# Optimization experiments

Hardware: AMD Instinct MI355X
Metric: run time of the kernel (lower is better)

## Reference

```python
import jax, jax.numpy as jnp
import numpy as np

IN, H, OUT, T, B = 132, 1024, 132, 100, 256


def setup_inputs() -> dict:
    key = jax.random.key(0)
    ks = jax.random.split(key, 16)
    s_in = 1.0 / np.sqrt(H)
    def mk(k, shape):
        return jax.random.uniform(k, shape, jnp.float32, -s_in, s_in)
    inp = {
        "real_seq": jax.random.normal(ks[0], (B, T, IN), jnp.float32),
        "W_ih1": mk(ks[1], (4 * H, IN)), "W_hh1": mk(ks[2], (4 * H, H)),
        "b_ih1": mk(ks[3], (4 * H,)),   "b_hh1": mk(ks[4], (4 * H,)),
        "W_ih2": mk(ks[5], (4 * H, H)), "W_hh2": mk(ks[6], (4 * H, H)),
        "b_ih2": mk(ks[7], (4 * H,)),   "b_hh2": mk(ks[8], (4 * H,)),
        "W_ih3": mk(ks[9], (4 * H, H)), "W_hh3": mk(ks[10], (4 * H, H)),
        "b_ih3": mk(ks[11], (4 * H,)),  "b_hh3": mk(ks[12], (4 * H,)),
        "W_dec": mk(ks[13], (OUT, H)),  "b_dec": mk(ks[14], (OUT,)),
        "condition_num": 5, "groundtruth_num": 5,
    }
    return inp


def _lstm_cell(x, h, c, W_ih, W_hh, b_ih, b_hh):
    # torch LSTMCell: gates in (i, f, g, o) order
    gates = x @ W_ih.T + b_ih + h @ W_hh.T + b_hh
    i, f, g, o = jnp.split(gates, 4, axis=-1)
    i, f, o = jax.nn.sigmoid(i), jax.nn.sigmoid(f), jax.nn.sigmoid(o)
    g = jnp.tanh(g)
    c_new = f * c + i * g
    h_new = o * jnp.tanh(c_new)
    return h_new, c_new


def reference(real_seq, W_ih1, W_hh1, b_ih1, b_hh1,
              W_ih2, W_hh2, b_ih2, b_hh2,
              W_ih3, W_hh3, b_ih3, b_hh3,
              W_dec, b_dec, condition_num, groundtruth_num):
    batch, seq_len, _ = real_seq.shape
    # static teacher-forcing schedule: [1]*gt_num + [0]*cond_num, tiled
    gt = np.ones((100, groundtruth_num)); con = np.zeros((100, condition_num))
    cond = jnp.asarray(np.concatenate((gt, con), 1).reshape(-1)[:seq_len] == 1)

    z = jnp.zeros((batch, H), jnp.float32)
    init = (z, z, z, z, z, z, jnp.zeros((batch, OUT), jnp.float32))

    def step(carry, xs):
        h0, h1, h2, c0, c1, c2, prev_out = carry
        frame, use_gt = xs
        x = jnp.where(use_gt, frame, prev_out)
        # note: lstm2/lstm3 consume the OLD h0/h1, faithful to forward_lstm
        nh0, nc0 = _lstm_cell(x,  h0, c0, W_ih1, W_hh1, b_ih1, b_hh1)
        nh1, nc1 = _lstm_cell(h0, h1, c1, W_ih2, W_hh2, b_ih2, b_hh2)
        nh2, nc2 = _lstm_cell(h1, h2, c2, W_ih3, W_hh3, b_ih3, b_hh3)
        out = nh2 @ W_dec.T + b_dec
        return (nh0, nh1, nh2, nc0, nc1, nc2, out), out

    xs = (jnp.swapaxes(real_seq, 0, 1), cond)  # [T,B,IN], [T]
    _, outs = jax.lax.scan(step, init, xs)      # outs: [T,B,OUT]
    # torch concatenates along dim 1 each step -> [B, T*OUT]
    return jnp.swapaxes(outs, 0, 1).reshape(batch, seq_len * OUT)
```

## Files before the change

### kernel.cpp

```cpp
#include <hip/hip_runtime.h>
#include <math.h>

#define B_   256
#define T_   100
#define IN_  132
#define OUT_ 132
#define H_   1024
#define BH   ((size_t)B_ * H_)

typedef _Float16 f16;
typedef _Float16 f16x8 __attribute__((ext_vector_type(8)));
typedef float    f32x4 __attribute__((ext_vector_type(4)));

#define MFMA16(a, b, c) __builtin_amdgcn_mfma_f32_16x16x32_f16((a), (b), (c), 0, 0, 0)

#define AS1 __attribute__((address_space(1)))
#define AS3 __attribute__((address_space(3)))

__device__ __forceinline__ void gl_lds16(const void* g, void* l) {
    __builtin_amdgcn_global_load_lds((AS1 void*)g, (AS3 void*)l, 16, 0, 0);
}

__device__ __forceinline__ float sigmoidf_(float x) {
    return 1.0f / (1.0f + __expf(-x));
}
__device__ __forceinline__ float tanhf_(float x) {
    float e = __expf(2.0f * x);
    return 1.0f - 2.0f / (e + 1.0f);
}


__global__ void conv_pad(const float* __restrict__ src, f16* __restrict__ dst,
                         int src_rows, int src_k, int dst_k) {
    int k = blockIdx.x * 256 + threadIdx.x;
    int r = blockIdx.y;
    if (k >= dst_k) return;
    float v = (r < src_rows && k < src_k) ? src[(size_t)r * src_k + k] : 0.0f;
    dst[(size_t)r * dst_k + k] = (f16)v;
}

__global__ void convT_kernel(const float* __restrict__ Wd, f16* __restrict__ WdT) {
    int k = blockIdx.x * 256 + threadIdx.x;
    int m = blockIdx.y;
    if (k >= 160) return;
    float v = (k < IN_) ? Wd[(size_t)k * H_ + m] : 0.0f;
    WdT[(size_t)m * 160 + k] = (f16)v;
}

__global__ void bias_add_kernel(const float* __restrict__ a, const float* __restrict__ b,
                                float* __restrict__ dst, int n) {
    int i = blockIdx.x * 256 + threadIdx.x;
    if (i < n) dst[i] = a[i] + b[i];
}

__global__ void bfb_kernel(const float* __restrict__ Wih1, const float* __restrict__ bd,
                           float* __restrict__ bfb) {
    int j = blockIdx.x * 256 + threadIdx.x;
    if (j >= 4096) return;
    float s = 0.0f;
    for (int k = 0; k < IN_; ++k) s += Wih1[(size_t)j * IN_ + k] * bd[k];
    bfb[j] = s;
}

__global__ void zero_kernel(float* __restrict__ p, int n) {
    int i = blockIdx.x * blockDim.x + threadIdx.x;
    int st = gridDim.x * blockDim.x;
    for (; i < n; i += st) p[i] = 0.0f;
}

__global__ __launch_bounds__(256) void pack_w(const float* __restrict__ W,
                                              f16* __restrict__ Wpk, int wsel) {
    int jt = blockIdx.x, kt = blockIdx.y;
    f16* dst = Wpk + (((size_t)wsel * 32 + jt) * 32 + kt) * 4096;
    for (int u = threadIdx.x; u < 512; u += 256) {
        int c = u >> 2, ch = u & 3;
        int gate = (c >> 4) & 3, jj = (c & 15) + (c >> 6) * 16;
        const float* s = W + ((size_t)gate * 1024 + jt * 32 + jj) * 1024 + kt * 32 + ch * 8;
        f16x8 v;
#pragma unroll
        for (int e = 0; e < 8; ++e) v[e] = (f16)s[e];
        *(f16x8*)(dst + (size_t)u * 8) = v;
    }
}

__global__ __launch_bounds__(256) void pack_wf16(const f16* __restrict__ W,
                                                 f16* __restrict__ Wpk, int wsel) {
    int jt = blockIdx.x, kt = blockIdx.y;
    f16* dst = Wpk + (((size_t)wsel * 32 + jt) * 32 + kt) * 4096;
    for (int u = threadIdx.x; u < 512; u += 256) {
        int c = u >> 2, ch = u & 3;
        int gate = (c >> 4) & 3, jj = (c & 15) + (c >> 6) * 16;
        const f16* s = W + ((size_t)gate * 1024 + jt * 32 + jj) * 1024 + kt * 32 + ch * 8;
        f16x8 v = *(const f16x8*)s;
        *(f16x8*)(dst + (size_t)u * 8) = v;
    }
}

__global__ __launch_bounds__(256) void pack_w0(const float* __restrict__ W,
                                               f16* __restrict__ W0pk) {
    int jt = blockIdx.x, kt = blockIdx.y;
    f16* dst = W0pk + ((size_t)jt * 5 + kt) * 4096;
    for (int u = threadIdx.x; u < 512; u += 256) {
        int c = u >> 2, ch = u & 3;
        int gate = (c >> 4) & 3, jj = (c & 15) + (c >> 6) * 16;
        int row = gate * 1024 + jt * 32 + jj;
        f16x8 v;
#pragma unroll
        for (int e = 0; e < 8; ++e) {
            int k = kt * 32 + ch * 8 + e;
            v[e] = (f16)((k < IN_) ? W[(size_t)row * IN_ + k] : 0.0f);
        }
        *(f16x8*)(dst + (size_t)u * 8) = v;
    }
}

__global__ __launch_bounds__(256) void pack_seq(const float* __restrict__ seq,
                                                f16* __restrict__ seqpk) {
    int kt = blockIdx.x, t = blockIdx.y;
    int b = threadIdx.x;
    f16* d = seqpk + (((size_t)t * 5 + kt) * 256 + b) * 32;
#pragma unroll
    for (int ch = 0; ch < 4; ++ch) {
        f16x8 v;
#pragma unroll
        for (int e = 0; e < 8; ++e) {
            int k = kt * 32 + ch * 8 + e;
            v[e] = (f16)((k < IN_) ? seq[((size_t)b * T_ + t) * IN_ + k] : 0.0f);
        }
        *(f16x8*)(d + ch * 8) = v;
    }
}

__global__ __launch_bounds__(256) void wfb_mfma(
    const f16* __restrict__ W0, const f16* __restrict__ WdT, f16* __restrict__ Wfb)
{
    const int m0 = blockIdx.x * 128;
    const int n0 = blockIdx.y * 128;
    const int tid  = threadIdx.x;
    const int lane = tid & 63;
    const int w    = tid >> 6;
    const int lx   = lane & 15;
    const int quad = lane >> 4;
    const int wrow = w >> 1, wcol = w & 1;

    __shared__ __align__(16) char lds[32768];

    auto stA = [&](int kt, int buf) {
        char* base = lds + buf * 16384;
#pragma unroll
        for (int i = 0; i < 2; ++i) {
            int r  = w * 32 + i * 16 + (lane >> 2);
            int sg = (lane & 3) ^ (r & 3);
            const f16* g = W0 + (size_t)(m0 + r) * 160 + kt * 32 + sg * 8;
            gl_lds16(g, base + (size_t)(w * 32 + i * 16) * 64);
        }
    };
    auto stB = [&](int kt, int buf) {
        char* base = lds + 8192 + buf * 16384;
#pragma unroll
        for (int i = 0; i < 2; ++i) {
            int r  = w * 32 + i * 16 + (lane >> 2);
            int sg = (lane & 3) ^ (r & 3);
            const f16* g = WdT + (size_t)(n0 + r) * 160 + kt * 32 + sg * 8;
            gl_lds16(g, base + (size_t)(w * 32 + i * 16) * 64);
        }
    };

    f32x4 acc[4][4];
#pragma unroll
    for (int m = 0; m < 4; ++m)
#pragma unroll
        for (int n = 0; n < 4; ++n) acc[m][n] = (f32x4){0.f, 0.f, 0.f, 0.f};

    stA(0, 0); stB(0, 0);
    for (int kt = 0; kt < 5; ++kt) {
        __syncthreads();
        if (kt + 1 < 5) { stA(kt + 1, (kt + 1) & 1); stB(kt + 1, (kt + 1) & 1); }
        const char* bA = lds + (kt & 1) * 16384;
        const char* bB = lds + 8192 + (kt & 1) * 16384;
        f16x8 af[4], bf[4];
#pragma unroll
        for (int m = 0; m < 4; ++m) {
            int R = wrow * 64 + m * 16 + lx;
            af[m] = *(const f16x8*)(bA + R * 64 + ((quad ^ (R & 3)) * 16));
        }
#pragma unroll
        for (int n = 0; n < 4; ++n) {
            int R = wcol * 64 + n * 16 + lx;
            bf[n] = *(const f16x8*)(bB + R * 64 + ((quad ^ (R & 3)) * 16));
        }
#pragma unroll
        for (int m = 0; m < 4; ++m)
#pragma unroll
            for (int n = 0; n < 4; ++n)
                acc[m][n] = MFMA16(af[m], bf[n], acc[m][n]);
    }

#pragma unroll
    for (int m = 0; m < 4; ++m)
#pragma unroll
        for (int n = 0; n < 4; ++n)
#pragma unroll
            for (int r = 0; r < 4; ++r) {
                int row = m0 + wrow * 64 + m * 16 + quad * 4 + r;
                int col = n0 + wcol * 64 + n * 16 + lx;
                Wfb[(size_t)row * H_ + col] = (f16)acc[m][n][r];
            }
}

__global__ __launch_bounds__(256) void step_mfma(
    const f16* __restrict__ seqpk,
    const f16* __restrict__ h2pkP,
    const f16* __restrict__ h01pkC,
    f16* __restrict__ h01pkN,
    f16* __restrict__ h2pkN,
    f16* __restrict__ histN,
    float* __restrict__ c_st,
    const f16* __restrict__ W0pk,
    const f16* __restrict__ Wpk,
    const float* __restrict__ bias_comb,
    const float* __restrict__ bfb,
    const int* __restrict__ cnum, const int* __restrict__ gnum,
    int t)
{
    const int jt   = blockIdx.x;
    const int mb   = blockIdx.y;
    const int l    = blockIdx.z;
    const int tid  = threadIdx.x;
    const int lane = tid & 63;
    const int w    = tid >> 6;
    const int lx   = lane & 15;
    const int quad = lane >> 4;
    const int wrow = w >> 1, wcol = w & 1;

    __shared__ __align__(16) char lds[49152];

    bool use_gt = false;
    int n0 = 32;
    const char *A0 = nullptr, *B0 = nullptr;
    const char* wb = (const char*)Wpk + (size_t)jt * 262144;
    if (l == 0) {
        int cn = cnum[0], gn = gnum[0];
        use_gt = (t % (cn + gn)) < gn;
        if (use_gt)      { A0 = (const char*)(seqpk + (size_t)t * 5 * 8192);
                           B0 = (const char*)(W0pk + (size_t)jt * 5 * 4096); n0 = 5; }
        else if (t == 0) { n0 = 0; }
        else             { A0 = (const char*)h2pkP; B0 = wb + (size_t)5 * 8388608; }
    } else if (l == 1) { A0 = (const char*)h01pkC;        B0 = wb + (size_t)1 * 8388608; }
    else               { A0 = (const char*)(h01pkC + BH); B0 = wb + (size_t)3 * 8388608; }
    const char* A1 = (l == 0) ? (const char*)h01pkC
                   : (l == 1) ? (const char*)(h01pkC + BH) : (const char*)h2pkP;
    const char* B1 = wb + (size_t)((l == 0) ? 0 : (l == 1) ? 2 : 4) * 8388608;
    const int ntot = n0 + 32;

    const int lr = lane >> 2, lc = lane & 3;
    const int perl = lr * 64 + ((lc ^ (lr & 3)) * 16);

    auto stage = [&](int kt, int buf) {
        const char *pA, *pB; int kk;
        if (kt < n0) { kk = kt;      pA = A0; pB = B0; }
        else         { kk = kt - n0; pA = A1; pB = B1; }
        char* base = lds + buf * 12288;
        gl_lds16(pA + (size_t)kk * 16384 + (size_t)(mb * 64 + w * 16) * 64 + perl,
                 base + w * 1024);
#pragma unroll
        for (int i = 0; i < 2; ++i)
            gl_lds16(pB + (size_t)kk * 8192 + (size_t)(w * 2 + i) * 1024 + perl,
                     base + 4096 + (size_t)(w * 2 + i) * 1024);
    };

    f32x4 acc[2][4];
#pragma unroll
    for (int m = 0; m < 2; ++m)
#pragma unroll
        for (int n = 0; n < 4; ++n) acc[m][n] = (f32x4){0.f, 0.f, 0.f, 0.f};

    stage(0, 0);
    stage(1, 1);
    stage(2, 2);

    for (int kt = 0; kt < ntot; ++kt) {
        if (kt < ntot - 2)       asm volatile("s_waitcnt vmcnt(6)" ::: "memory");
        else if (kt == ntot - 2) asm volatile("s_waitcnt vmcnt(3)" ::: "memory");
        else                     asm volatile("s_waitcnt vmcnt(0)" ::: "memory");
        __builtin_amdgcn_s_barrier();

        const char* bA = lds + (kt & 3) * 12288;
        const char* bB = bA + 4096;
        f16x8 af[2], bf[4];
#pragma unroll
        for (int m = 0; m < 2; ++m) {
            int R = wrow * 32 + m * 16 + lx;
            af[m] = *(const f16x8*)(bA + R * 64 + ((quad ^ (R & 3)) * 16));
        }
#pragma unroll
        for (int n = 0; n < 4; ++n) {
            int R = wcol * 64 + n * 16 + lx;
            bf[n] = *(const f16x8*)(bB + R * 64 + ((quad ^ (R & 3)) * 16));
        }
        asm volatile("s_waitcnt lgkmcnt(0)" ::: "memory");
        __builtin_amdgcn_sched_barrier(0);
        __builtin_amdgcn_s_barrier();

        if (kt + 3 < ntot) stage(kt + 3, (kt + 3) & 3);

        __builtin_amdgcn_s_setprio(1);
#pragma unroll
        for (int m = 0; m < 2; ++m)
#pragma unroll
            for (int n = 0; n < 4; ++n)
                acc[m][n] = MFMA16(af[m], bf[n], acc[m][n]);
        __builtin_amdgcn_s_setprio(0);
    }

    const int j = jt * 32 + wcol * 16 + lx;
    const float* bc = bias_comb + l * 4096;
    const bool addfb = (l == 0 && !use_gt && t > 0);
    float bi  = bc[j]        + (addfb ? bfb[j]        : 0.f);
    float bff = bc[1024 + j] + (addfb ? bfb[1024 + j] : 0.f);
    float bg  = bc[2048 + j] + (addfb ? bfb[2048 + j] : 0.f);
    float bo  = bc[3072 + j] + (addfb ? bfb[3072 + j] : 0.f);
#pragma unroll
    for (int m = 0; m < 2; ++m) {
#pragma unroll
        for (int r = 0; r < 4; ++r) {
            int b = mb * 64 + wrow * 32 + m * 16 + quad * 4 + r;
            float gi = acc[m][0][r] + bi;
            float gf = acc[m][1][r] + bff;
            float gg = acc[m][2][r] + bg;
            float go = acc[m][3][r] + bo;
            size_t ix = ((size_t)l * B_ + b) * H_ + j;
            float cn = sigmoidf_(gf) * c_st[ix] + sigmoidf_(gi) * tanhf_(gg);
            c_st[ix] = cn;
            float hv = sigmoidf_(go) * tanhf_(cn);
            f16 hv16 = (f16)hv;
            size_t pix = ((size_t)(j >> 5) * 256 + b) * 32 + (j & 31);
            if (l == 2) { h2pkN[pix] = hv16; histN[(size_t)b * H_ + j] = hv16; }
            else        h01pkN[(size_t)l * BH + pix] = hv16;
        }
    }
}

__global__ __launch_bounds__(256) void decode_mfma(
    const f16* __restrict__ hist,
    const f16* __restrict__ Wd16,
    const float* __restrict__ bd,
    float* __restrict__ dout)
{
    const int r0  = blockIdx.x * 128;
    const int nb0 = blockIdx.y * 32;
    const int tid  = threadIdx.x;
    const int lane = tid & 63;
    const int w    = tid >> 6;
    const int lx   = lane & 15;
    const int quad = lane >> 4;

    __shared__ __align__(16) char lds[20480];

    auto stA = [&](int kt, int buf) {
        char* base = lds + buf * 10240;
#pragma unroll
        for (int i = 0; i < 2; ++i) {
            int r  = w * 32 + i * 16 + (lane >> 2);
            int sg = (lane & 3) ^ (r & 3);
            const f16* g = hist + (size_t)(r0 + r) * H_ + kt * 32 + sg * 8;
            gl_lds16(g, base + (size_t)(w * 32 + i * 16) * 64);
        }
    };
    auto stB = [&](int kt, int buf) {
        char* base = lds + 8192 + buf * 10240;
        if (w < 2) {
            int r  = w * 16 + (lane >> 2);
            int sg = (lane & 3) ^ (r & 3);
            const f16* g = Wd16 + (size_t)(nb0 + r) * H_ + kt * 32 + sg * 8;
            gl_lds16(g, base + (size_t)(w * 16) * 64);
        }
    };

    f32x4 acc[2][2];
#pragma unroll
    for (int m = 0; m < 2; ++m)
#pragma unroll
        for (int n = 0; n < 2; ++n) acc[m][n] = (f32x4){0.f, 0.f, 0.f, 0.f};

    stA(0, 0); stB(0, 0);
    for (int kt = 0; kt < 32; ++kt) {
        __syncthreads();
        if (kt + 1 < 32) { stA(kt + 1, (kt + 1) & 1); stB(kt + 1, (kt + 1) & 1); }
        const char* bA = lds + (kt & 1) * 10240;
        const char* bB = lds + 8192 + (kt & 1) * 10240;
        f16x8 af[2], bf[2];
#pragma unroll
        for (int m = 0; m < 2; ++m) {
            int R = w * 32 + m * 16 + lx;
            af[m] = *(const f16x8*)(bA + R * 64 + ((quad ^ (R & 3)) * 16));
        }
#pragma unroll
        for (int n = 0; n < 2; ++n) {
            int R = n * 16 + lx;
            bf[n] = *(const f16x8*)(bB + R * 64 + ((quad ^ (R & 3)) * 16));
        }
#pragma unroll
        for (int m = 0; m < 2; ++m)
#pragma unroll
            for (int n = 0; n < 2; ++n)
                acc[m][n] = MFMA16(af[m], bf[n], acc[m][n]);
    }

#pragma unroll
    for (int n = 0; n < 2; ++n) {
        int nn = nb0 + n * 16 + lx;
        if (nn < OUT_) {
            float bv = bd[nn];
#pragma unroll
            for (int m = 0; m < 2; ++m)
#pragma unroll
                for (int r = 0; r < 4; ++r) {
                    int row = r0 + w * 32 + m * 16 + quad * 4 + r;
                    int tt = row >> 8, b = row & 255;
                    dout[(size_t)b * (T_ * OUT_) + (size_t)tt * OUT_ + nn] = acc[m][n][r] + bv;
                }
        }
    }
}


extern "C" void kernel_launch(void* const* d_in, const int* in_sizes, int n_in,
                              void* d_out, int out_size, void* d_ws, size_t ws_size,
                              hipStream_t stream) {
    const float* seq  = (const float*)d_in[0];
    const float* Wih1 = (const float*)d_in[1];
    const float* Whh1 = (const float*)d_in[2];
    const float* bih1 = (const float*)d_in[3];
    const float* bhh1 = (const float*)d_in[4];
    const float* Wih2 = (const float*)d_in[5];
    const float* Whh2 = (const float*)d_in[6];
    const float* bih2 = (const float*)d_in[7];
    const float* bhh2 = (const float*)d_in[8];
    const float* Wih3 = (const float*)d_in[9];
    const float* Whh3 = (const float*)d_in[10];
    const float* bih3 = (const float*)d_in[11];
    const float* bhh3 = (const float*)d_in[12];
    const float* Wd   = (const float*)d_in[13];
    const float* bd   = (const float*)d_in[14];
    const int*   cnum = (const int*)d_in[15];
    const int*   gnum = (const int*)d_in[16];

    char* p = (char*)d_ws;
    f16*  W0   = (f16*)p;  p += (size_t)4096 * 160 * 2;
    f16*  Wd16 = (f16*)p;  p += (size_t)160 * 1024 * 2;
    f16*  WdT  = (f16*)p;  p += (size_t)1024 * 160 * 2;
    f16*  Wfb  = (f16*)p;  p += (size_t)4096 * 1024 * 2;
    float* bias_comb = (float*)p; p += (size_t)3 * 4096 * 4;
    float* bfb = (float*)p; p += (size_t)4096 * 4;
    f16*  hist = (f16*)p;  p += (size_t)100 * BH * 2;
    f16*  h01pkA = (f16*)p; p += (size_t)2 * BH * 2;
    f16*  h2pkA  = (f16*)p; p += (size_t)BH * 2;
    float* c_st  = (float*)p; p += (size_t)3 * BH * 4;
    f16*  h01pkB = (f16*)p; p += (size_t)2 * BH * 2;
    f16*  h2pkB  = (f16*)p; p += (size_t)BH * 2;
    f16*  Wpk   = (f16*)p; p += (size_t)6 * 32 * 32 * 4096 * 2;
    f16*  W0pk  = (f16*)p; p += (size_t)32 * 5 * 4096 * 2;
    f16*  seqpk = (f16*)p; p += (size_t)T_ * 5 * 256 * 32 * 2;

    const int zero_floats = (int)(((size_t)3 * BH * 2 + (size_t)3 * BH * 4) / 4);

    conv_pad<<<dim3(1, 4096), 256, 0, stream>>>(Wih1, W0, 4096, IN_, 160);
    conv_pad<<<dim3(4, 160), 256, 0, stream>>>(Wd, Wd16, OUT_, H_, H_);
    convT_kernel<<<dim3(1, 1024), 256, 0, stream>>>(Wd, WdT);
    bias_add_kernel<<<16, 256, 0, stream>>>(bih1, bhh1, bias_comb + 0 * 4096, 4096);
    bias_add_kernel<<<16, 256, 0, stream>>>(bih2, bhh2, bias_comb + 1 * 4096, 4096);
    bias_add_kernel<<<16, 256, 0, stream>>>(bih3, bhh3, bias_comb + 2 * 4096, 4096);
    bfb_kernel<<<16, 256, 0, stream>>>(Wih1, bd, bfb);
    wfb_mfma<<<dim3(32, 8), 256, 0, stream>>>(W0, WdT, Wfb);
    pack_w<<<dim3(32, 32), 256, 0, stream>>>(Whh1, Wpk, 0);
    pack_w<<<dim3(32, 32), 256, 0, stream>>>(Wih2, Wpk, 1);
    pack_w<<<dim3(32, 32), 256, 0, stream>>>(Whh2, Wpk, 2);
    pack_w<<<dim3(32, 32), 256, 0, stream>>>(Wih3, Wpk, 3);
    pack_w<<<dim3(32, 32), 256, 0, stream>>>(Whh3, Wpk, 4);
    pack_wf16<<<dim3(32, 32), 256, 0, stream>>>(Wfb, Wpk, 5);
    pack_w0<<<dim3(32, 5), 256, 0, stream>>>(Wih1, W0pk);
    pack_seq<<<dim3(5, T_), 256, 0, stream>>>(seq, seqpk);
    zero_kernel<<<512, 256, 0, stream>>>((float*)h01pkA, zero_floats);

    f16 *h01C = h01pkA, *h01N = h01pkB, *h2P = h2pkA, *h2N = h2pkB;
    for (int t = 0; t < T_; ++t) {
        step_mfma<<<dim3(32, 4, 3), 256, 0, stream>>>(
            seqpk, h2P, h01C, h01N, h2N, hist + (size_t)t * BH, c_st,
            W0pk, Wpk, bias_comb, bfb, cnum, gnum, t);
        f16* tmp;
        tmp = h01C; h01C = h01N; h01N = tmp;
        tmp = h2P;  h2P  = h2N;  h2N  = tmp;
    }

    decode_mfma<<<dim3(200, 5), 256, 0, stream>>>(hist, Wd16, bd, (float*)d_out);
}
```

Baseline: 3.020 ms.

## Split step kernel K-dimension across two waves with register-direct loads

```diff
diff --git a/kernel.cpp b/kernel.cpp
--- a/kernel.cpp
+++ b/kernel.cpp
@@ -70,48 +70,43 @@
 
 __global__ __launch_bounds__(256) void pack_w(const float* __restrict__ W,
                                               f16* __restrict__ Wpk, int wsel) {
-    int jt = blockIdx.x, kt = blockIdx.y;
-    f16* dst = Wpk + (((size_t)wsel * 32 + jt) * 32 + kt) * 4096;
-    for (int u = threadIdx.x; u < 512; u += 256) {
-        int c = u >> 2, ch = u & 3;
-        int gate = (c >> 4) & 3, jj = (c & 15) + (c >> 6) * 16;
-        const float* s = W + ((size_t)gate * 1024 + jt * 32 + jj) * 1024 + kt * 32 + ch * 8;
-        f16x8 v;
-#pragma unroll
-        for (int e = 0; e < 8; ++e) v[e] = (f16)s[e];
-        *(f16x8*)(dst + (size_t)u * 8) = v;
-    }
+    int jt = blockIdx.x, kk = blockIdx.y;
+    f16* dst = Wpk + (((size_t)wsel * 64 + jt) * 32 + kk) * 2048;
+    int u = threadIdx.x;
+    int c = u >> 2, ch = u & 3;
+    int row = ((c >> 4) & 3) * 1024 + jt * 16 + (c & 15);
+    const float* s = W + (size_t)row * 1024 + kk * 32 + ch * 8;
+    f16x8 v;
+#pragma unroll
+    for (int e = 0; e < 8; ++e) v[e] = (f16)s[e];
+    *(f16x8*)(dst + (size_t)c * 32 + ch * 8) = v;
 }
 
 __global__ __launch_bounds__(256) void pack_wf16(const f16* __restrict__ W,
                                                  f16* __restrict__ Wpk, int wsel) {
-    int jt = blockIdx.x, kt = blockIdx.y;
-    f16* dst = Wpk + (((size_t)wsel * 32 + jt) * 32 + kt) * 4096;
-    for (int u = threadIdx.x; u < 512; u += 256) {
-        int c = u >> 2, ch = u & 3;
-        int gate = (c >> 4) & 3, jj = (c & 15) + (c >> 6) * 16;
-        const f16* s = W + ((size_t)gate * 1024 + jt * 32 + jj) * 1024 + kt * 32 + ch * 8;
-        f16x8 v = *(const f16x8*)s;
-        *(f16x8*)(dst + (size_t)u * 8) = v;
-    }
+    int jt = blockIdx.x, kk = blockIdx.y;
+    f16* dst = Wpk + (((size_t)wsel * 64 + jt) * 32 + kk) * 2048;
+    int u = threadIdx.x;
+    int c = u >> 2, ch = u & 3;
+    int row = ((c >> 4) & 3) * 1024 + jt * 16 + (c & 15);
+    f16x8 v = *(const f16x8*)(W + (size_t)row * 1024 + kk * 32 + ch * 8);
+    *(f16x8*)(dst + (size_t)c * 32 + ch * 8) = v;
 }
 
 __global__ __launch_bounds__(256) void pack_w0(const float* __restrict__ W,
                                                f16* __restrict__ W0pk) {
-    int jt = blockIdx.x, kt = blockIdx.y;
-    f16* dst = W0pk + ((size_t)jt * 5 + kt) * 4096;
-    for (int u = threadIdx.x; u < 512; u += 256) {
-        int c = u >> 2, ch = u & 3;
-        int gate = (c >> 4) & 3, jj = (c & 15) + (c >> 6) * 16;
-        int row = gate * 1024 + jt * 32 + jj;
-        f16x8 v;
-#pragma unroll
-        for (int e = 0; e < 8; ++e) {
-            int k = kt * 32 + ch * 8 + e;
-            v[e] = (f16)((k < IN_) ? W[(size_t)row * IN_ + k] : 0.0f);
-        }
-        *(f16x8*)(dst + (size_t)u * 8) = v;
-    }
+    int jt = blockIdx.x, kk = blockIdx.y;
+    f16* dst = W0pk + ((size_t)jt * 5 + kk) * 2048;
+    int u = threadIdx.x;
+    int c = u >> 2, ch = u & 3;
+    int row = ((c >> 4) & 3) * 1024 + jt * 16 + (c & 15);
+    f16x8 v;
+#pragma unroll
+    for (int e = 0; e < 8; ++e) {
+        int k = kk * 32 + ch * 8 + e;
+        v[e] = (f16)((k < IN_) ? W[(size_t)row * IN_ + k] : 0.0f);
+    }
+    *(f16x8*)(dst + (size_t)c * 32 + ch * 8) = v;
 }
 
 __global__ __launch_bounds__(256) void pack_seq(const float* __restrict__ seq,
@@ -208,7 +203,7 @@
             }
 }
 
-__global__ __launch_bounds__(256) void step_mfma(
+__global__ __launch_bounds__(128) void step_mfma(
     const f16* __restrict__ seqpk,
     const f16* __restrict__ h2pkP,
     const f16* __restrict__ h01pkC,
@@ -231,89 +226,95 @@
     const int w    = tid >> 6;
     const int lx   = lane & 15;
     const int quad = lane >> 4;
-    const int wrow = w >> 1, wcol = w & 1;
-
-    __shared__ __align__(16) char lds[49152];
+
+    __shared__ float ex[2][2][4][4][64];
 
     bool use_gt = false;
     int n0 = 32;
     const char *A0 = nullptr, *B0 = nullptr;
-    const char* wb = (const char*)Wpk + (size_t)jt * 262144;
+    const char* wbase = (const char*)Wpk + (size_t)jt * 131072;
     if (l == 0) {
         int cn = cnum[0], gn = gnum[0];
         use_gt = (t % (cn + gn)) < gn;
-        if (use_gt)      { A0 = (const char*)(seqpk + (size_t)t * 5 * 8192);
-                           B0 = (const char*)(W0pk + (size_t)jt * 5 * 4096); n0 = 5; }
+        if (use_gt)      { A0 = (const char*)(seqpk + (size_t)t * 40960);
+                           B0 = (const char*)(W0pk + (size_t)jt * 10240); n0 = 5; }
         else if (t == 0) { n0 = 0; }
-        else             { A0 = (const char*)h2pkP; B0 = wb + (size_t)5 * 8388608; }
-    } else if (l == 1) { A0 = (const char*)h01pkC;        B0 = wb + (size_t)1 * 8388608; }
-    else               { A0 = (const char*)(h01pkC + BH); B0 = wb + (size_t)3 * 8388608; }
+        else             { A0 = (const char*)h2pkP; B0 = wbase + (size_t)5 * 8388608; }
+    } else if (l == 1) { A0 = (const char*)h01pkC;        B0 = wbase + (size_t)1 * 8388608; }
+    else               { A0 = (const char*)(h01pkC + BH); B0 = wbase + (size_t)3 * 8388608; }
     const char* A1 = (l == 0) ? (const char*)h01pkC
                    : (l == 1) ? (const char*)(h01pkC + BH) : (const char*)h2pkP;
-    const char* B1 = wb + (size_t)((l == 0) ? 0 : (l == 1) ? 2 : 4) * 8388608;
+    const char* B1 = wbase + (size_t)((l == 0) ? 0 : (l == 1) ? 2 : 4) * 8388608;
     const int ntot = n0 + 32;
-
-    const int lr = lane >> 2, lc = lane & 3;
-    const int perl = lr * 64 + ((lc ^ (lr & 3)) * 16);
-
-    auto stage = [&](int kt, int buf) {
-        const char *pA, *pB; int kk;
-        if (kt < n0) { kk = kt;      pA = A0; pB = B0; }
-        else         { kk = kt - n0; pA = A1; pB = B1; }
-        char* base = lds + buf * 12288;
-        gl_lds16(pA + (size_t)kk * 16384 + (size_t)(mb * 64 + w * 16) * 64 + perl,
-                 base + w * 1024);
-#pragma unroll
-        for (int i = 0; i < 2; ++i)
-            gl_lds16(pB + (size_t)kk * 8192 + (size_t)(w * 2 + i) * 1024 + perl,
-                     base + 4096 + (size_t)(w * 2 + i) * 1024);
-    };
-
-    f32x4 acc[2][4];
-#pragma unroll
-    for (int m = 0; m < 2; ++m)
+    const int nh = (ntot + 1) >> 1;
+    const int lo = w ? nh : 0;
+    const int hi = w ? ntot : nh;
+
+    const int aoff = (mb * 64 + lx) * 64 + quad * 16;
+    const int boff = lx * 64 + quad * 16;
+
+    f32x4 acc[4][4];
+#pragma unroll
+    for (int m = 0; m < 4; ++m)
 #pragma unroll
         for (int n = 0; n < 4; ++n) acc[m][n] = (f32x4){0.f, 0.f, 0.f, 0.f};
 
-    stage(0, 0);
-    stage(1, 1);
-    stage(2, 2);
-
-    for (int kt = 0; kt < ntot; ++kt) {
-        if (kt < ntot - 2)       asm volatile("s_waitcnt vmcnt(6)" ::: "memory");
-        else if (kt == ntot - 2) asm volatile("s_waitcnt vmcnt(3)" ::: "memory");
-        else                     asm volatile("s_waitcnt vmcnt(0)" ::: "memory");
-        __builtin_amdgcn_s_barrier();
-
-        const char* bA = lds + (kt & 3) * 12288;
-        const char* bB = bA + 4096;
-        f16x8 af[2], bf[4];
-#pragma unroll
-        for (int m = 0; m < 2; ++m) {
-            int R = wrow * 32 + m * 16 + lx;
-            af[m] = *(const f16x8*)(bA + R * 64 + ((quad ^ (R & 3)) * 16));
-        }
-#pragma unroll
-        for (int n = 0; n < 4; ++n) {
-            int R = wcol * 64 + n * 16 + lx;
-            bf[n] = *(const f16x8*)(bB + R * 64 + ((quad ^ (R & 3)) * 16));
-        }
-        asm volatile("s_waitcnt lgkmcnt(0)" ::: "memory");
-        __builtin_amdgcn_sched_barrier(0);
-        __builtin_amdgcn_s_barrier();
-
-        if (kt + 3 < ntot) stage(kt + 3, (kt + 3) & 3);
-
-        __builtin_amdgcn_s_setprio(1);
-#pragma unroll
-        for (int m = 0; m < 2; ++m)
+    f16x8 a0[4], b0[4], a1r[4], b1r[4];
+
+    auto LD = [&](f16x8 (&aa)[4], f16x8 (&bb)[4], int it) {
+        int kk; const char *pa, *pb;
+        if (it < n0) { kk = it;      pa = A0; pb = B0; }
+        else         { kk = it - n0; pa = A1; pb = B1; }
+        pa += (size_t)kk * 16384 + aoff;
+        pb += (size_t)kk * 4096 + boff;
+#pragma unroll
+        for (int m = 0; m < 4; ++m) aa[m] = *(const f16x8*)(pa + m * 1024);
+#pragma unroll
+        for (int n = 0; n < 4; ++n) bb[n] = *(const f16x8*)(pb + n * 1024);
+    };
+    auto MF = [&](f16x8 (&aa)[4], f16x8 (&bb)[4]) {
+#pragma unroll
+        for (int m = 0; m < 4; ++m)
 #pragma unroll
             for (int n = 0; n < 4; ++n)
-                acc[m][n] = MFMA16(af[m], bf[n], acc[m][n]);
-        __builtin_amdgcn_s_setprio(0);
-    }
-
-    const int j = jt * 32 + wcol * 16 + lx;
+                acc[m][n] = MFMA16(aa[m], bb[n], acc[m][n]);
+    };
+
+    int it = lo;
+    if (it < hi) LD(a0, b0, it);
+    for (; it + 2 <= hi; it += 2) {
+        LD(a1r, b1r, it + 1);
+        MF(a0, b0);
+        if (it + 2 < hi) LD(a0, b0, it + 2);
+        MF(a1r, b1r);
+    }
+    if (it < hi) MF(a0, b0);
+
+#pragma unroll
+    for (int m2 = 0; m2 < 2; ++m2)
+#pragma unroll
+        for (int n = 0; n < 4; ++n)
+#pragma unroll
+            for (int r = 0; r < 4; ++r) {
+                if (w == 1) ex[0][m2][n][r][lane] = acc[m2][n][r];
+                else        ex[1][m2][n][r][lane] = acc[2 + m2][n][r];
+            }
+    __syncthreads();
+
+    f32x4 fa[2][4];
+    if (w == 0) {
+#pragma unroll
+        for (int m2 = 0; m2 < 2; ++m2)
+#pragma unroll
+            for (int n = 0; n < 4; ++n) fa[m2][n] = acc[m2][n];
+    } else {
+#pragma unroll
+        for (int m2 = 0; m2 < 2; ++m2)
+#pragma unroll
+            for (int n = 0; n < 4; ++n) fa[m2][n] = acc[2 + m2][n];
+    }
+
+    const int j = jt * 16 + lx;
     const float* bc = bias_comb + l * 4096;
     const bool addfb = (l == 0 && !use_gt && t > 0);
     float bi  = bc[j]        + (addfb ? bfb[j]        : 0.f);
@@ -321,14 +322,14 @@
     float bg  = bc[2048 + j] + (addfb ? bfb[2048 + j] : 0.f);
     float bo  = bc[3072 + j] + (addfb ? bfb[3072 + j] : 0.f);
 #pragma unroll
-    for (int m = 0; m < 2; ++m) {
+    for (int m2 = 0; m2 < 2; ++m2) {
 #pragma unroll
         for (int r = 0; r < 4; ++r) {
-            int b = mb * 64 + wrow * 32 + m * 16 + quad * 4 + r;
-            float gi = acc[m][0][r] + bi;
-            float gf = acc[m][1][r] + bff;
-            float gg = acc[m][2][r] + bg;
-            float go = acc[m][3][r] + bo;
+            int b = mb * 64 + (w * 2 + m2) * 16 + quad * 4 + r;
+            float gi = fa[m2][0][r] + ex[w][m2][0][r][lane] + bi;
+            float gf = fa[m2][1][r] + ex[w][m2][1][r][lane] + bff;
+            float gg = fa[m2][2][r] + ex[w][m2][2][r][lane] + bg;
+            float go = fa[m2][3][r] + ex[w][m2][3][r][lane] + bo;
             size_t ix = ((size_t)l * B_ + b) * H_ + j;
             float cn = sigmoidf_(gf) * c_st[ix] + sigmoidf_(gi) * tanhf_(gg);
             c_st[ix] = cn;
@@ -459,8 +460,8 @@
     float* c_st  = (float*)p; p += (size_t)3 * BH * 4;
     f16*  h01pkB = (f16*)p; p += (size_t)2 * BH * 2;
     f16*  h2pkB  = (f16*)p; p += (size_t)BH * 2;
-    f16*  Wpk   = (f16*)p; p += (size_t)6 * 32 * 32 * 4096 * 2;
-    f16*  W0pk  = (f16*)p; p += (size_t)32 * 5 * 4096 * 2;
+    f16*  Wpk   = (f16*)p; p += (size_t)6 * 64 * 32 * 2048 * 2;
+    f16*  W0pk  = (f16*)p; p += (size_t)64 * 5 * 2048 * 2;
     f16*  seqpk = (f16*)p; p += (size_t)T_ * 5 * 256 * 32 * 2;
 
     const int zero_floats = (int)(((size_t)3 * BH * 2 + (size_t)3 * BH * 4) / 4);
@@ -473,19 +474,19 @@
     bias_add_kernel<<<16, 256, 0, stream>>>(bih3, bhh3, bias_comb + 2 * 4096, 4096);
     bfb_kernel<<<16, 256, 0, stream>>>(Wih1, bd, bfb);
     wfb_mfma<<<dim3(32, 8), 256, 0, stream>>>(W0, WdT, Wfb);
-    pack_w<<<dim3(32, 32), 256, 0, stream>>>(Whh1, Wpk, 0);
-    pack_w<<<dim3(32, 32), 256, 0, stream>>>(Wih2, Wpk, 1);
-    pack_w<<<dim3(32, 32), 256, 0, stream>>>(Whh2, Wpk, 2);
-    pack_w<<<dim3(32, 32), 256, 0, stream>>>(Wih3, Wpk, 3);
-    pack_w<<<dim3(32, 32), 256, 0, stream>>>(Whh3, Wpk, 4);
-    pack_wf16<<<dim3(32, 32), 256, 0, stream>>>(Wfb, Wpk, 5);
-    pack_w0<<<dim3(32, 5), 256, 0, stream>>>(Wih1, W0pk);
+    pack_w<<<dim3(64, 32), 256, 0, stream>>>(Whh1, Wpk, 0);
+    pack_w<<<dim3(64, 32), 256, 0, stream>>>(Wih2, Wpk, 1);
+    pack_w<<<dim3(64, 32), 256, 0, stream>>>(Whh2, Wpk, 2);
+    pack_w<<<dim3(64, 32), 256, 0, stream>>>(Wih3, Wpk, 3);
+    pack_w<<<dim3(64, 32), 256, 0, stream>>>(Whh3, Wpk, 4);
+    pack_wf16<<<dim3(64, 32), 256, 0, stream>>>(Wfb, Wpk, 5);
+    pack_w0<<<dim3(64, 5), 256, 0, stream>>>(Wih1, W0pk);
     pack_seq<<<dim3(5, T_), 256, 0, stream>>>(seq, seqpk);
     zero_kernel<<<512, 256, 0, stream>>>((float*)h01pkA, zero_floats);
 
     f16 *h01C = h01pkA, *h01N = h01pkB, *h2P = h2pkA, *h2N = h2pkB;
     for (int t = 0; t < T_; ++t) {
-        step_mfma<<<dim3(32, 4, 3), 256, 0, stream>>>(
+        step_mfma<<<dim3(64, 4, 3), 128, 0, stream>>>(
             seqpk, h2P, h01C, h01N, h2N, hist + (size_t)t * BH, c_st,
             W0pk, Wpk, bias_comb, bfb, cnum, gnum, t);
         f16* tmp;
```

Result: no change. 3.030 ms (+0.3%).
